# Optimization experiments

Measured on AMD Instinct MI355X. Metric: run time of the kernel, lower is better.

Reference implementation:

```python
import jax, jax.numpy as jnp
import numpy as np


def _ternary(x, delta):
    # {-1, 0, +1} thresholded at +/- delta
    return jnp.where(x > delta, 1.0, jnp.where(x < -delta, -1.0, 0.0)).astype(x.dtype)


def setup_inputs() -> dict:
    key = jax.random.key(0)
    kx, kw = jax.random.split(key)
    x = jax.random.normal(kx, (8192, 4096), dtype=jnp.float32)
    weight = jax.random.normal(kw, (4096, 4096), dtype=jnp.float32) * 0.02
    return {"x": x, "weight": weight}


def reference(x, weight):
    # TernaryActivation: delta = 0.1 * mean|x|
    x_q = _ternary(x, 0.1 * jnp.mean(jnp.abs(x)))
    # TernaryQuantize: delta = 0.05 * mean|w|, scaled by alpha = mean|w|
    w_abs_mean = jnp.mean(jnp.abs(weight))
    w_q = w_abs_mean * _ternary(weight, 0.05 * w_abs_mean)
    # F.linear(x_q, w_q) = x_q @ w_q.T
    return jnp.einsum('bi,oi->bo', x_q, w_q)
```

## Files before the change

### kernel.cpp

```cpp
#include <hip/hip_runtime.h>
#include <stdint.h>

typedef __attribute__((ext_vector_type(4))) int i32x4;
typedef __attribute__((ext_vector_type(16))) float f32x16;

#define MROWS 8192L
#define NCOLS 4096L
#define KDIM  4096L

#define XQ_BYTES   (MROWS * KDIM / 2)
#define WQ_BYTES   (NCOLS * KDIM / 2)
#define SCAL_OFF   (XQ_BYTES + WQ_BYTES)

__global__ __launch_bounds__(256) void k_reduce_abs(const float* __restrict__ x,
                                                    const float* __restrict__ w,
                                                    float* __restrict__ partials) {
    __shared__ float sm[256];
    int b = blockIdx.x;
    int t = threadIdx.x;
    const float4* v;
    long base;
    if (b < 512) { v = (const float4*)x; base = (long)b * 16384; }
    else         { v = (const float4*)w; base = (long)(b - 512) * 16384; }
    float s = 0.f;
    for (int i = t; i < 16384; i += 256) {
        float4 q = v[base + i];
        s += fabsf(q.x) + fabsf(q.y) + fabsf(q.z) + fabsf(q.w);
    }
    sm[t] = s;
    __syncthreads();
    for (int off = 128; off > 0; off >>= 1) {
        if (t < off) sm[t] += sm[t + off];
        __syncthreads();
    }
    if (t == 0) partials[b] = sm[0];
}

__global__ __launch_bounds__(256) void k_finalize(float* __restrict__ scal) {
    const float* partials = scal + 4;
    __shared__ double sm[256];
    int t = threadIdx.x;

    double sx = 0.0;
    for (int i = t; i < 512; i += 256) sx += (double)partials[i];
    sm[t] = sx;
    __syncthreads();
    for (int off = 128; off > 0; off >>= 1) {
        if (t < off) sm[t] += sm[t + off];
        __syncthreads();
    }
    double SX = sm[0];
    __syncthreads();

    double sw = (double)partials[512 + t];
    sm[t] = sw;
    __syncthreads();
    for (int off = 128; off > 0; off >>= 1) {
        if (t < off) sm[t] += sm[t + off];
        __syncthreads();
    }
    if (t == 0) {
        float meanx = (float)(SX / 33554432.0);
        float meanw = (float)(sm[0] / 16777216.0);
        scal[0] = 0.1f * meanx;
        scal[1] = 0.05f * meanw;
        scal[2] = meanw;
    }
}

__device__ __forceinline__ unsigned int nib4(float v, float delta) {
    return v > delta ? 2u : (v < -delta ? 10u : 0u);
}

__global__ __launch_bounds__(256) void k_quantF(const float* __restrict__ x,
                                                const float* __restrict__ w,
                                                uint4* __restrict__ xq,
                                                uint4* __restrict__ wq,
                                                const float* __restrict__ scal) {
    int wv = blockIdx.x * 4 + (threadIdx.x >> 6);
    int l = threadIdx.x & 63;

    const float* src;
    uint4* dst;
    float delta;
    int task;
    if (wv < 16384) {
        src = x; dst = xq; delta = scal[0]; task = wv;
    } else {
        src = w; dst = wq; delta = scal[1]; task = wv - 16384;
    }
    int rowblk = task >> 6;
    int rest = task & 63;
    long row = (long)rowblk * 32 + (l & 31);
    long fidx = row * 4096 + (long)(rest >> 1) * 128 + (long)(rest & 1) * 64
              + (long)(l >> 5) * 32;
    const float4* s4 = (const float4*)(src + fidx);

    unsigned int ow[4];
#pragma unroll
    for (int c = 0; c < 4; ++c) {
        float4 q0 = s4[2 * c];
        float4 q1 = s4[2 * c + 1];
        ow[c] = nib4(q0.x, delta)
              | (nib4(q0.y, delta) << 4)
              | (nib4(q0.z, delta) << 8)
              | (nib4(q0.w, delta) << 12)
              | (nib4(q1.x, delta) << 16)
              | (nib4(q1.y, delta) << 20)
              | (nib4(q1.z, delta) << 24)
              | (nib4(q1.w, delta) << 28);
    }
    uint4 o; o.x = ow[0]; o.y = ow[1]; o.z = ow[2]; o.w = ow[3];
    dst[(long)task * 64 + l] = o;
}

#define GLOAD_LDS16(g, l)                                                             \
    __builtin_amdgcn_global_load_lds((const __attribute__((address_space(1))) void*)(g), \
                                     (__attribute__((address_space(3))) void*)(l),       \
                                     16, 0, 0)

#define MK8(v) __builtin_shufflevector((v), (v), 0, 1, 2, 3, -1, -1, -1, -1)

#define MFMA32(a, b, c)                                                       \
    __builtin_amdgcn_mfma_scale_f32_32x32x64_f8f6f4(MK8(a), MK8(b), (c),      \
        4, 4, 0, 0x7F7F7F7F, 0, 0x7F7F7F7F)

__global__ __launch_bounds__(512, 2) void k_gemm(const signed char* __restrict__ Xq,
                                                 const signed char* __restrict__ Wq,
                                                 float* __restrict__ out,
                                                 const float* __restrict__ scal) {
    __shared__ __attribute__((aligned(16))) signed char lds[131072];

    const float alpha = scal[2];

    int bid = (int)blockIdx.x;
    bid = (bid & 7) * 64 + (bid >> 3);
    int bm = bid >> 4;
    int bn = bid & 15;
    long row0 = (long)bm * 256;
    long col0 = (long)bn * 256;

    int t = threadIdx.x;
    int lane = t & 63;
    int wid = t >> 6;
    int wm = wid >> 2;
    int wn = wid & 3;

    const signed char* sp[4];
    int ldoff[4];
#pragma unroll
    for (int j = 0; j < 4; ++j) {
        int g = wid * 4 + j;
        ldoff[j] = g * 1024;
        if (g < 16) {
            long rowblk = bm * 8 + (g >> 3) * 4 + ((g >> 1) & 3);
            sp[j] = Xq + rowblk * 65536 + (g & 1) * 1024 + lane * 16;
        } else {
            int h = g - 16;
            long colblk = bn * 8 + (h >> 2) * 2 + ((h >> 1) & 1);
            sp[j] = Wq + colblk * 65536 + (h & 1) * 1024 + lane * 16;
        }
    }

#define STAGE(slot, g1) do {                                                   \
    signed char* sb_ = lds + (slot) * 32768;                                   \
    _Pragma("unroll")                                                          \
    for (int j_ = 0; j_ < 4; ++j_)                                             \
        GLOAD_LDS16(sp[j_] + (long)(g1) * 2048, sb_ + ldoff[j_]);              \
} while (0)

    const signed char* Ab = lds + wm * 8192 + lane * 16;
    const signed char* Bb = lds + 16384 + wn * 4096 + lane * 16;

    f32x16 acc[4][2];
#pragma unroll
    for (int i = 0; i < 4; ++i)
#pragma unroll
        for (int j = 0; j < 2; ++j)
            acc[i][j] = (f32x16){0.f};

#define BODY(slot) do {                                                        \
    const signed char* A = Ab + (slot) * 32768;                                \
    const signed char* B = Bb + (slot) * 32768;                                \
    i32x4 b00 = *(const i32x4*)(B + 0 * 1024);                                 \
    i32x4 b10 = *(const i32x4*)(B + 2 * 1024);                                 \
    i32x4 a00 = *(const i32x4*)(A + 0 * 1024);                                 \
    i32x4 a10 = *(const i32x4*)(A + 2 * 1024);                                 \
    acc[0][0] = MFMA32(a00, b00, acc[0][0]);                                   \
    acc[1][0] = MFMA32(a10, b00, acc[1][0]);                                   \
    acc[0][1] = MFMA32(a00, b10, acc[0][1]);                                   \
    acc[1][1] = MFMA32(a10, b10, acc[1][1]);                                   \
    i32x4 b01 = *(const i32x4*)(B + 1 * 1024);                                 \
    i32x4 b11 = *(const i32x4*)(B + 3 * 1024);                                 \
    i32x4 a01 = *(const i32x4*)(A + 1 * 1024);                                 \
    i32x4 a11 = *(const i32x4*)(A + 3 * 1024);                                 \
    acc[0][0] = MFMA32(a01, b01, acc[0][0]);                                   \
    acc[1][0] = MFMA32(a11, b01, acc[1][0]);                                   \
    acc[0][1] = MFMA32(a01, b11, acc[0][1]);                                   \
    acc[1][1] = MFMA32(a11, b11, acc[1][1]);                                   \
    i32x4 a20 = *(const i32x4*)(A + 4 * 1024);                                 \
    i32x4 a30 = *(const i32x4*)(A + 6 * 1024);                                 \
    acc[2][0] = MFMA32(a20, b00, acc[2][0]);                                   \
    acc[3][0] = MFMA32(a30, b00, acc[3][0]);                                   \
    acc[2][1] = MFMA32(a20, b10, acc[2][1]);                                   \
    acc[3][1] = MFMA32(a30, b10, acc[3][1]);                                   \
    i32x4 a21 = *(const i32x4*)(A + 5 * 1024);                                 \
    i32x4 a31 = *(const i32x4*)(A + 7 * 1024);                                 \
    acc[2][0] = MFMA32(a21, b01, acc[2][0]);                                   \
    acc[3][0] = MFMA32(a31, b01, acc[3][0]);                                   \
    acc[2][1] = MFMA32(a21, b11, acc[2][1]);                                   \
    acc[3][1] = MFMA32(a31, b11, acc[3][1]);                                   \
} while (0)

    STAGE(0, 0);
    STAGE(1, 1);

    for (int d = 0; d < 16; ++d) {
        int s0 = (2 * d) & 3;
        int s1 = (2 * d + 1) & 3;
        __builtin_amdgcn_s_barrier();
        if (d < 15) {
            STAGE((2 * d + 2) & 3, 2 * d + 2);
            STAGE((2 * d + 3) & 3, 2 * d + 3);
            asm volatile("s_waitcnt vmcnt(8)" ::: "memory");
        } else {
            asm volatile("s_waitcnt vmcnt(0)" ::: "memory");
        }
        __builtin_amdgcn_s_barrier();
        __builtin_amdgcn_sched_barrier(0);

        BODY(s0);
        BODY(s1);
    }

#pragma unroll
    for (int mi = 0; mi < 4; ++mi) {
#pragma unroll
        for (int ni = 0; ni < 2; ++ni) {
            long col = col0 + wn * 64 + ni * 32 + (lane & 31);
            long rowb = row0 + wm * 128 + mi * 32 + 4 * (lane >> 5);
#pragma unroll
            for (int r = 0; r < 16; ++r) {
                long row = rowb + (r & 3) + 8 * (r >> 2);
                out[row * NCOLS + col] = alpha * acc[mi][ni][r];
            }
        }
    }
#undef BODY
#undef STAGE
}

extern "C" void kernel_launch(void* const* d_in, const int* in_sizes, int n_in,
                              void* d_out, int out_size, void* d_ws, size_t ws_size,
                              hipStream_t stream) {
    const float* x = (const float*)d_in[0];
    const float* w = (const float*)d_in[1];
    float* out = (float*)d_out;

    uint8_t* ws = (uint8_t*)d_ws;
    signed char* Xq = (signed char*)ws;
    signed char* Wq = (signed char*)(ws + XQ_BYTES);
    float* scal = (float*)(ws + SCAL_OFF);

    k_reduce_abs<<<768, 256, 0, stream>>>(x, w, scal + 4);
    k_finalize<<<1, 256, 0, stream>>>(scal);
    k_quantF<<<6144, 256, 0, stream>>>(x, w, (uint4*)Xq, (uint4*)Wq, scal);
    k_gemm<<<512, 512, 0, stream>>>(Xq, Wq, out, scal);
}
```

Baseline: 153.8 us.

## Load B operand directly to registers, shrink LDS to double-buffered A only

The GEMM kernel no longer stages the weight (B) tile through LDS. Each wave loads its B fragments straight from global memory into registers, double-buffered across k-steps, while only the activation (A) tile is staged in LDS with a two-slot buffer. This cuts LDS from 128KB to 32KB and removes the B LDS reads, with the goal of better occupancy and lower LDS traffic. It also adds s_setprio around the MFMA bodies. In exchange, B loads become redundant across the two wm waves, prefetch depth falls from four slots to two, and the vmcnt accounting gets more fragile.

```diff
diff --git a/kernel.cpp b/kernel.cpp
--- a/kernel.cpp
+++ b/kernel.cpp
@@ -129,7 +129,7 @@
                                                  const signed char* __restrict__ Wq,
                                                  float* __restrict__ out,
                                                  const float* __restrict__ scal) {
-    __shared__ __attribute__((aligned(16))) signed char lds[131072];
+    __shared__ __attribute__((aligned(16))) signed char lds[32768];
 
     const float alpha = scal[2];
 
@@ -146,31 +146,28 @@
     int wm = wid >> 2;
     int wn = wid & 3;
 
-    const signed char* sp[4];
-    int ldoff[4];
-#pragma unroll
-    for (int j = 0; j < 4; ++j) {
-        int g = wid * 4 + j;
-        ldoff[j] = g * 1024;
-        if (g < 16) {
-            long rowblk = bm * 8 + (g >> 3) * 4 + ((g >> 1) & 3);
-            sp[j] = Xq + rowblk * 65536 + (g & 1) * 1024 + lane * 16;
-        } else {
-            int h = g - 16;
-            long colblk = bn * 8 + (h >> 2) * 2 + ((h >> 1) & 1);
-            sp[j] = Wq + colblk * 65536 + (h & 1) * 1024 + lane * 16;
-        }
-    }
-
-#define STAGE(slot, g1) do {                                                   \
-    signed char* sb_ = lds + (slot) * 32768;                                   \
-    _Pragma("unroll")                                                          \
-    for (int j_ = 0; j_ < 4; ++j_)                                             \
-        GLOAD_LDS16(sp[j_] + (long)(g1) * 2048, sb_ + ldoff[j_]);              \
+    const signed char* sp[2];
+    int ldoff[2];
+#pragma unroll
+    for (int j = 0; j < 2; ++j) {
+        int ga = wid * 2 + j;
+        ldoff[j] = ga * 1024;
+        sp[j] = Xq + (long)(bm * 8 + (ga >> 1)) * 65536 + (ga & 1) * 1024 + lane * 16;
+    }
+
+#define STAGE_A(slot, g1) do {                                                 \
+    signed char* sb_ = lds + (slot) * 16384;                                   \
+    GLOAD_LDS16(sp[0] + (long)(g1) * 2048, sb_ + ldoff[0]);                    \
+    GLOAD_LDS16(sp[1] + (long)(g1) * 2048, sb_ + ldoff[1]);                    \
 } while (0)
 
-    const signed char* Ab = lds + wm * 8192 + lane * 16;
-    const signed char* Bb = lds + 16384 + wn * 4096 + lane * 16;
+    const signed char* pb0 = Wq + (long)(bn * 8 + wn * 2 + 0) * 65536 + 0 * 1024 + lane * 16;
+    const signed char* pb1 = Wq + (long)(bn * 8 + wn * 2 + 1) * 65536 + 0 * 1024 + lane * 16;
+    const signed char* pb2 = Wq + (long)(bn * 8 + wn * 2 + 0) * 65536 + 1 * 1024 + lane * 16;
+    const signed char* pb3 = Wq + (long)(bn * 8 + wn * 2 + 1) * 65536 + 1 * 1024 + lane * 16;
+#define LDB(p, off) (*(const i32x4*)((p) + (off)))
+
+    const signed char* Aw = lds + wm * 8192 + lane * 16;
 
     f32x16 acc[4][2];
 #pragma unroll
@@ -179,58 +176,66 @@
         for (int j = 0; j < 2; ++j)
             acc[i][j] = (f32x16){0.f};
 
-#define BODY(slot) do {                                                        \
-    const signed char* A = Ab + (slot) * 32768;                                \
-    const signed char* B = Bb + (slot) * 32768;                                \
-    i32x4 b00 = *(const i32x4*)(B + 0 * 1024);                                 \
-    i32x4 b10 = *(const i32x4*)(B + 2 * 1024);                                 \
+#define BODY(slot, B0, B1, B2, B3) do {                                        \
+    const signed char* A = Aw + (slot) * 16384;                                \
     i32x4 a00 = *(const i32x4*)(A + 0 * 1024);                                 \
     i32x4 a10 = *(const i32x4*)(A + 2 * 1024);                                 \
-    acc[0][0] = MFMA32(a00, b00, acc[0][0]);                                   \
-    acc[1][0] = MFMA32(a10, b00, acc[1][0]);                                   \
-    acc[0][1] = MFMA32(a00, b10, acc[0][1]);                                   \
-    acc[1][1] = MFMA32(a10, b10, acc[1][1]);                                   \
-    i32x4 b01 = *(const i32x4*)(B + 1 * 1024);                                 \
-    i32x4 b11 = *(const i32x4*)(B + 3 * 1024);                                 \
+    acc[0][0] = MFMA32(a00, B0, acc[0][0]);                                    \
+    acc[0][1] = MFMA32(a00, B1, acc[0][1]);                                    \
+    acc[1][0] = MFMA32(a10, B0, acc[1][0]);                                    \
+    acc[1][1] = MFMA32(a10, B1, acc[1][1]);                                    \
+    i32x4 a20 = *(const i32x4*)(A + 4 * 1024);                                 \
+    i32x4 a30 = *(const i32x4*)(A + 6 * 1024);                                 \
+    acc[2][0] = MFMA32(a20, B0, acc[2][0]);                                    \
+    acc[2][1] = MFMA32(a20, B1, acc[2][1]);                                    \
+    acc[3][0] = MFMA32(a30, B0, acc[3][0]);                                    \
+    acc[3][1] = MFMA32(a30, B1, acc[3][1]);                                    \
     i32x4 a01 = *(const i32x4*)(A + 1 * 1024);                                 \
     i32x4 a11 = *(const i32x4*)(A + 3 * 1024);                                 \
-    acc[0][0] = MFMA32(a01, b01, acc[0][0]);                                   \
-    acc[1][0] = MFMA32(a11, b01, acc[1][0]);                                   \
-    acc[0][1] = MFMA32(a01, b11, acc[0][1]);                                   \
-    acc[1][1] = MFMA32(a11, b11, acc[1][1]);                                   \
-    i32x4 a20 = *(const i32x4*)(A + 4 * 1024);                                 \
-    i32x4 a30 = *(const i32x4*)(A + 6 * 1024);                                 \
-    acc[2][0] = MFMA32(a20, b00, acc[2][0]);                                   \
-    acc[3][0] = MFMA32(a30, b00, acc[3][0]);                                   \
-    acc[2][1] = MFMA32(a20, b10, acc[2][1]);                                   \
-    acc[3][1] = MFMA32(a30, b10, acc[3][1]);                                   \
+    acc[0][0] = MFMA32(a01, B2, acc[0][0]);                                    \
+    acc[0][1] = MFMA32(a01, B3, acc[0][1]);                                    \
+    acc[1][0] = MFMA32(a11, B2, acc[1][0]);                                    \
+    acc[1][1] = MFMA32(a11, B3, acc[1][1]);                                    \
     i32x4 a21 = *(const i32x4*)(A + 5 * 1024);                                 \
     i32x4 a31 = *(const i32x4*)(A + 7 * 1024);                                 \
-    acc[2][0] = MFMA32(a21, b01, acc[2][0]);                                   \
-    acc[3][0] = MFMA32(a31, b01, acc[3][0]);                                   \
-    acc[2][1] = MFMA32(a21, b11, acc[2][1]);                                   \
-    acc[3][1] = MFMA32(a31, b11, acc[3][1]);                                   \
+    acc[2][0] = MFMA32(a21, B2, acc[2][0]);                                    \
+    acc[2][1] = MFMA32(a21, B3, acc[2][1]);                                    \
+    acc[3][0] = MFMA32(a31, B2, acc[3][0]);                                    \
+    acc[3][1] = MFMA32(a31, B3, acc[3][1]);                                    \
 } while (0)
 
-    STAGE(0, 0);
-    STAGE(1, 1);
+    STAGE_A(0, 0);
+    i32x4 e0 = LDB(pb0, 0), e1 = LDB(pb1, 0), e2 = LDB(pb2, 0), e3 = LDB(pb3, 0);
+    i32x4 o0, o1, o2, o3;
 
     for (int d = 0; d < 16; ++d) {
-        int s0 = (2 * d) & 3;
-        int s1 = (2 * d + 1) & 3;
+        int g0 = 2 * d;
+        __builtin_amdgcn_s_barrier();
+        {
+            STAGE_A(1, g0 + 1);
+            long kn = (long)(g0 + 1) * 2048;
+            o0 = LDB(pb0, kn); o1 = LDB(pb1, kn); o2 = LDB(pb2, kn); o3 = LDB(pb3, kn);
+            asm volatile("s_waitcnt vmcnt(6)" ::: "memory");
+        }
+        __builtin_amdgcn_s_barrier();
+        __builtin_amdgcn_sched_barrier(0);
+        __builtin_amdgcn_s_setprio(1);
+        BODY(0, e0, e1, e2, e3);
+        __builtin_amdgcn_s_setprio(0);
         __builtin_amdgcn_s_barrier();
         if (d < 15) {
-            STAGE((2 * d + 2) & 3, 2 * d + 2);
-            STAGE((2 * d + 3) & 3, 2 * d + 3);
-            asm volatile("s_waitcnt vmcnt(8)" ::: "memory");
+            STAGE_A(0, g0 + 2);
+            long kn = (long)(g0 + 2) * 2048;
+            e0 = LDB(pb0, kn); e1 = LDB(pb1, kn); e2 = LDB(pb2, kn); e3 = LDB(pb3, kn);
+            asm volatile("s_waitcnt vmcnt(6)" ::: "memory");
         } else {
             asm volatile("s_waitcnt vmcnt(0)" ::: "memory");
         }
         __builtin_amdgcn_s_barrier();
         __builtin_amdgcn_sched_barrier(0);
-
-        BODY(s0);
-        BODY(s1);
+        __builtin_amdgcn_s_setprio(1);
+        BODY(1, o0, o1, o2, o3);
+        __builtin_amdgcn_s_setprio(0);
     }
 
 #pragma unroll
@@ -247,7 +252,8 @@
         }
     }
 #undef BODY
-#undef STAGE
+#undef LDB
+#undef STAGE_A
 }
 
 extern "C" void kernel_launch(void* const* d_in, const int* in_sizes, int n_in,
```

Result: slower. 165.0 us (+7.3%).

## Split GEMM into two half-grid kernels with different pipelining schedules

Applied to the files above, without the earlier changes.

The single GEMM launch becomes two kernels, each covering half the row blocks. Kernel A keeps the original double-stage loop and raises wave priority around the MFMA bodies. Kernel B interleaves one global-to-LDS load per MFMA phase, with barriers and waitcnts between phases, for finer-grained overlap. This looks like an A/B comparison of schedules, and it adds an extra launch that halves the grid per kernel and may leave CUs underused.

```diff
diff --git a/kernel.cpp b/kernel.cpp
--- a/kernel.cpp
+++ b/kernel.cpp
@@ -125,61 +125,74 @@
     __builtin_amdgcn_mfma_scale_f32_32x32x64_f8f6f4(MK8(a), MK8(b), (c),      \
         4, 4, 0, 0x7F7F7F7F, 0, 0x7F7F7F7F)
 
-__global__ __launch_bounds__(512, 2) void k_gemm(const signed char* __restrict__ Xq,
-                                                 const signed char* __restrict__ Wq,
-                                                 float* __restrict__ out,
-                                                 const float* __restrict__ scal) {
-    __shared__ __attribute__((aligned(16))) signed char lds[131072];
-
-    const float alpha = scal[2];
-
-    int bid = (int)blockIdx.x;
-    bid = (bid & 7) * 64 + (bid >> 3);
-    int bm = bid >> 4;
-    int bn = bid & 15;
-    long row0 = (long)bm * 256;
-    long col0 = (long)bn * 256;
-
-    int t = threadIdx.x;
-    int lane = t & 63;
-    int wid = t >> 6;
-    int wm = wid >> 2;
-    int wn = wid & 3;
-
-    const signed char* sp[4];
-    int ldoff[4];
-#pragma unroll
-    for (int j = 0; j < 4; ++j) {
-        int g = wid * 4 + j;
-        ldoff[j] = g * 1024;
-        if (g < 16) {
-            long rowblk = bm * 8 + (g >> 3) * 4 + ((g >> 1) & 3);
-            sp[j] = Xq + rowblk * 65536 + (g & 1) * 1024 + lane * 16;
-        } else {
-            int h = g - 16;
-            long colblk = bn * 8 + (h >> 2) * 2 + ((h >> 1) & 1);
-            sp[j] = Wq + colblk * 65536 + (h & 1) * 1024 + lane * 16;
-        }
-    }
-
-#define STAGE(slot, g1) do {                                                   \
+#define GEMM_SETUP()                                                           \
+    const float alpha = scal[2];                                               \
+    int bid = (int)blockIdx.x;                                                 \
+    bid = (bid & 7) * 32 + (bid >> 3);            \
+    int bm = bm_base + (bid >> 4);                    \
+    int bn = bid & 15;                                                         \
+    long row0 = (long)bm * 256;                                                \
+    long col0 = (long)bn * 256;                                                \
+    int t = threadIdx.x;                                                       \
+    int lane = t & 63;                                                         \
+    int wid = t >> 6;                                                          \
+    int wm = wid >> 2;                                                         \
+    int wn = wid & 3;                                                          \
+    const signed char* sp[4];                                                  \
+    int ldoff[4];                                                              \
+    _Pragma("unroll")                                                          \
+    for (int j = 0; j < 4; ++j) {                                              \
+        int g = wid * 4 + j;                                                   \
+        ldoff[j] = g * 1024;                                                   \
+        if (g < 16) {                                                          \
+            long rowblk = bm * 8 + (g >> 3) * 4 + ((g >> 1) & 3);              \
+            sp[j] = Xq + rowblk * 65536 + (g & 1) * 1024 + lane * 16;          \
+        } else {                                                               \
+            int h = g - 16;                                                    \
+            long colblk = bn * 8 + (h >> 2) * 2 + ((h >> 1) & 1);              \
+            sp[j] = Wq + colblk * 65536 + (h & 1) * 1024 + lane * 16;          \
+        }                                                                      \
+    }                                                                          \
+    const signed char* Ab = lds + wm * 8192 + lane * 16;                       \
+    const signed char* Bb = lds + 16384 + wn * 4096 + lane * 16;               \
+    f32x16 acc[4][2];                                                          \
+    _Pragma("unroll")                                                          \
+    for (int i = 0; i < 4; ++i)                                                \
+        _Pragma("unroll")                                                      \
+        for (int j = 0; j < 2; ++j)                                            \
+            acc[i][j] = (f32x16){0.f};
+
+#define GEMM_EPILOGUE()                                                        \
+    _Pragma("unroll")                                                          \
+    for (int mi = 0; mi < 4; ++mi) {                                           \
+        _Pragma("unroll")                                                      \
+        for (int ni = 0; ni < 2; ++ni) {                                       \
+            long col = col0 + wn * 64 + ni * 32 + (lane & 31);                 \
+            long rowb = row0 + wm * 128 + mi * 32 + 4 * (lane >> 5);           \
+            _Pragma("unroll")                                                  \
+            for (int r = 0; r < 16; ++r) {                                     \
+                long row = rowb + (r & 3) + 8 * (r >> 2);                      \
+                out[row * NCOLS + col] = alpha * acc[mi][ni][r];               \
+            }                                                                  \
+        }                                                                      \
+    }
+
+#define STAGE4(slot, g1) do {                                                  \
     signed char* sb_ = lds + (slot) * 32768;                                   \
     _Pragma("unroll")                                                          \
     for (int j_ = 0; j_ < 4; ++j_)                                             \
         GLOAD_LDS16(sp[j_] + (long)(g1) * 2048, sb_ + ldoff[j_]);              \
 } while (0)
 
-    const signed char* Ab = lds + wm * 8192 + lane * 16;
-    const signed char* Bb = lds + 16384 + wn * 4096 + lane * 16;
-
-    f32x16 acc[4][2];
-#pragma unroll
-    for (int i = 0; i < 4; ++i)
-#pragma unroll
-        for (int j = 0; j < 2; ++j)
-            acc[i][j] = (f32x16){0.f};
-
-#define BODY(slot) do {                                                        \
+__global__ __launch_bounds__(512, 2) void k_gemmA(const signed char* __restrict__ Xq,
+                                                  const signed char* __restrict__ Wq,
+                                                  float* __restrict__ out,
+                                                  const float* __restrict__ scal,
+                                                  int bm_base) {
+    __shared__ __attribute__((aligned(16))) signed char lds[131072];
+    GEMM_SETUP();
+
+#define BODYA(slot) do {                                                       \
     const signed char* A = Ab + (slot) * 32768;                                \
     const signed char* B = Bb + (slot) * 32768;                                \
     i32x4 b00 = *(const i32x4*)(B + 0 * 1024);                                 \
@@ -212,42 +225,163 @@
     acc[3][1] = MFMA32(a31, b11, acc[3][1]);                                   \
 } while (0)
 
-    STAGE(0, 0);
-    STAGE(1, 1);
+    STAGE4(0, 0);
+    STAGE4(1, 1);
 
     for (int d = 0; d < 16; ++d) {
         int s0 = (2 * d) & 3;
         int s1 = (2 * d + 1) & 3;
         __builtin_amdgcn_s_barrier();
         if (d < 15) {
-            STAGE((2 * d + 2) & 3, 2 * d + 2);
-            STAGE((2 * d + 3) & 3, 2 * d + 3);
+            STAGE4((2 * d + 2) & 3, 2 * d + 2);
+            STAGE4((2 * d + 3) & 3, 2 * d + 3);
             asm volatile("s_waitcnt vmcnt(8)" ::: "memory");
         } else {
             asm volatile("s_waitcnt vmcnt(0)" ::: "memory");
         }
         __builtin_amdgcn_s_barrier();
         __builtin_amdgcn_sched_barrier(0);
-
-        BODY(s0);
-        BODY(s1);
-    }
-
-#pragma unroll
-    for (int mi = 0; mi < 4; ++mi) {
-#pragma unroll
-        for (int ni = 0; ni < 2; ++ni) {
-            long col = col0 + wn * 64 + ni * 32 + (lane & 31);
-            long rowb = row0 + wm * 128 + mi * 32 + 4 * (lane >> 5);
-#pragma unroll
-            for (int r = 0; r < 16; ++r) {
-                long row = rowb + (r & 3) + 8 * (r >> 2);
-                out[row * NCOLS + col] = alpha * acc[mi][ni][r];
-            }
-        }
-    }
-#undef BODY
-#undef STAGE
+        __builtin_amdgcn_s_setprio(1);
+        BODYA(s0);
+        BODYA(s1);
+        __builtin_amdgcn_s_setprio(0);
+    }
+    GEMM_EPILOGUE();
+#undef BODYA
+}
+
+#define PH_PRE() do {                                        \
+    __builtin_amdgcn_s_barrier();                            \
+    asm volatile("s_waitcnt lgkmcnt(0)" ::: "memory");       \
+    __builtin_amdgcn_sched_barrier(0);                       \
+    __builtin_amdgcn_s_setprio(1); } while (0)
+#define PH_POST() do {                                       \
+    __builtin_amdgcn_s_setprio(0);                           \
+    __builtin_amdgcn_s_barrier(); } while (0)
+#define PH_POST_V() do {                                     \
+    __builtin_amdgcn_s_setprio(0);                           \
+    asm volatile("s_waitcnt vmcnt(4)" ::: "memory");         \
+    __builtin_amdgcn_s_barrier(); } while (0)
+
+__global__ __launch_bounds__(512, 2) void k_gemmB(const signed char* __restrict__ Xq,
+                                                  const signed char* __restrict__ Wq,
+                                                  float* __restrict__ out,
+                                                  const float* __restrict__ scal,
+                                                  int bm_base) {
+    __shared__ __attribute__((aligned(16))) signed char lds[131072];
+    GEMM_SETUP();
+
+    STAGE4(0, 0);
+    STAGE4(1, 1);
+    asm volatile("s_waitcnt vmcnt(4)" ::: "memory");
+    __builtin_amdgcn_s_barrier();
+
+    for (int d = 0; d < 16; ++d) {
+        int s0 = (2 * d) & 3;
+        int s1 = (2 * d + 1) & 3;
+        int tg0 = (2 * d + 2) & 31;
+        int tg1 = (2 * d + 3) & 31;
+        int sl0 = (2 * d + 2) & 3;
+        int sl1 = (2 * d + 3) & 3;
+        signed char* sb0 = lds + sl0 * 32768;
+        signed char* sb1 = lds + sl1 * 32768;
+
+        const signed char* A = Ab + s0 * 32768;
+        const signed char* B = Bb + s0 * 32768;
+        i32x4 a00, a10, a20, a30, a01, a11, a21, a31, b00, b10, b01, b11;
+
+        b00 = *(const i32x4*)(B + 0 * 1024);
+        b10 = *(const i32x4*)(B + 2 * 1024);
+        a00 = *(const i32x4*)(A + 0 * 1024);
+        a10 = *(const i32x4*)(A + 2 * 1024);
+        GLOAD_LDS16(sp[0] + (long)tg0 * 2048, sb0 + ldoff[0]);
+        PH_PRE();
+        acc[0][0] = MFMA32(a00, b00, acc[0][0]);
+        acc[1][0] = MFMA32(a10, b00, acc[1][0]);
+        acc[0][1] = MFMA32(a00, b10, acc[0][1]);
+        acc[1][1] = MFMA32(a10, b10, acc[1][1]);
+        PH_POST();
+
+        b01 = *(const i32x4*)(B + 1 * 1024);
+        b11 = *(const i32x4*)(B + 3 * 1024);
+        a01 = *(const i32x4*)(A + 1 * 1024);
+        a11 = *(const i32x4*)(A + 3 * 1024);
+        GLOAD_LDS16(sp[1] + (long)tg0 * 2048, sb0 + ldoff[1]);
+        PH_PRE();
+        acc[0][0] = MFMA32(a01, b01, acc[0][0]);
+        acc[1][0] = MFMA32(a11, b01, acc[1][0]);
+        acc[0][1] = MFMA32(a01, b11, acc[0][1]);
+        acc[1][1] = MFMA32(a11, b11, acc[1][1]);
+        PH_POST();
+
+        a20 = *(const i32x4*)(A + 4 * 1024);
+        a30 = *(const i32x4*)(A + 6 * 1024);
+        GLOAD_LDS16(sp[2] + (long)tg0 * 2048, sb0 + ldoff[2]);
+        PH_PRE();
+        acc[2][0] = MFMA32(a20, b00, acc[2][0]);
+        acc[3][0] = MFMA32(a30, b00, acc[3][0]);
+        acc[2][1] = MFMA32(a20, b10, acc[2][1]);
+        acc[3][1] = MFMA32(a30, b10, acc[3][1]);
+        PH_POST();
+
+        a21 = *(const i32x4*)(A + 5 * 1024);
+        a31 = *(const i32x4*)(A + 7 * 1024);
+        GLOAD_LDS16(sp[3] + (long)tg0 * 2048, sb0 + ldoff[3]);
+        PH_PRE();
+        acc[2][0] = MFMA32(a21, b01, acc[2][0]);
+        acc[3][0] = MFMA32(a31, b01, acc[3][0]);
+        acc[2][1] = MFMA32(a21, b11, acc[2][1]);
+        acc[3][1] = MFMA32(a31, b11, acc[3][1]);
+        PH_POST_V();
+
+        A = Ab + s1 * 32768;
+        B = Bb + s1 * 32768;
+
+        b00 = *(const i32x4*)(B + 0 * 1024);
+        b10 = *(const i32x4*)(B + 2 * 1024);
+        a00 = *(const i32x4*)(A + 0 * 1024);
+        a10 = *(const i32x4*)(A + 2 * 1024);
+        GLOAD_LDS16(sp[0] + (long)tg1 * 2048, sb1 + ldoff[0]);
+        PH_PRE();
+        acc[0][0] = MFMA32(a00, b00, acc[0][0]);
+        acc[1][0] = MFMA32(a10, b00, acc[1][0]);
+        acc[0][1] = MFMA32(a00, b10, acc[0][1]);
+        acc[1][1] = MFMA32(a10, b10, acc[1][1]);
+        PH_POST();
+
+        b01 = *(const i32x4*)(B + 1 * 1024);
+        b11 = *(const i32x4*)(B + 3 * 1024);
+        a01 = *(const i32x4*)(A + 1 * 1024);
+        a11 = *(const i32x4*)(A + 3 * 1024);
+        GLOAD_LDS16(sp[1] + (long)tg1 * 2048, sb1 + ldoff[1]);
+        PH_PRE();
+        acc[0][0] = MFMA32(a01, b01, acc[0][0]);
+        acc[1][0] = MFMA32(a11, b01, acc[1][0]);
+        acc[0][1] = MFMA32(a01, b11, acc[0][1]);
+        acc[1][1] = MFMA32(a11, b11, acc[1][1]);
+        PH_POST();
+
+        a20 = *(const i32x4*)(A + 4 * 1024);
+        a30 = *(const i32x4*)(A + 6 * 1024);
+        GLOAD_LDS16(sp[2] + (long)tg1 * 2048, sb1 + ldoff[2]);
+        PH_PRE();
+        acc[2][0] = MFMA32(a20, b00, acc[2][0]);
+        acc[3][0] = MFMA32(a30, b00, acc[3][0]);
+        acc[2][1] = MFMA32(a20, b10, acc[2][1]);
+        acc[3][1] = MFMA32(a30, b10, acc[3][1]);
+        PH_POST();
+
+        a21 = *(const i32x4*)(A + 5 * 1024);
+        a31 = *(const i32x4*)(A + 7 * 1024);
+        GLOAD_LDS16(sp[3] + (long)tg1 * 2048, sb1 + ldoff[3]);
+        PH_PRE();
+        acc[2][0] = MFMA32(a21, b01, acc[2][0]);
+        acc[3][0] = MFMA32(a31, b01, acc[3][0]);
+        acc[2][1] = MFMA32(a21, b11, acc[2][1]);
+        acc[3][1] = MFMA32(a31, b11, acc[3][1]);
+        PH_POST_V();
+    }
+    GEMM_EPILOGUE();
 }
 
 extern "C" void kernel_launch(void* const* d_in, const int* in_sizes, int n_in,
@@ -265,5 +399,6 @@
     k_reduce_abs<<<768, 256, 0, stream>>>(x, w, scal + 4);
     k_finalize<<<1, 256, 0, stream>>>(scal);
     k_quantF<<<6144, 256, 0, stream>>>(x, w, (uint4*)Xq, (uint4*)Wq, scal);
-    k_gemm<<<512, 512, 0, stream>>>(Xq, Wq, out, scal);
-}
+    k_gemmA<<<256, 512, 0, stream>>>(Xq, Wq, out, scal, 0);
+    k_gemmB<<<256, 512, 0, stream>>>(Xq, Wq, out, scal, 16);
+}
```

Result: no change. 154.2 us (+0.3%).
